# Kernel tuning notes

Hardware: AMD Instinct MI355X
Metric: run time of the kernel (lower is better)

The kernel has to match this reference:

```python
import jax, jax.numpy as jnp
import numpy as np
import math

B, S, D, H, L = 16, 1024, 256, 8, 4
OBS, ACT = 160, 96
DH = D // H  # 32, even as required by RoPE
ROPE_BASE = 10000.0
LN_EPS = 1e-5


def setup_inputs() -> dict:
    key = jax.random.key(0)
    ks = jax.random.split(key, 16)
    s = 0.02
    n = jax.random.normal
    return {
        "obs_seq": n(ks[0], (B, S, OBS), jnp.float32),
        "action_seq": n(ks[1], (B, S, ACT), jnp.float32),
        # linears stored as [in, out] (transpose of torch convention)
        "in_W": n(ks[2], (OBS + ACT, D), jnp.float32) * s,
        "in_b": jnp.zeros((D,), jnp.float32),
        "qW": n(ks[3], (L, D, D), jnp.float32) * s,
        "qb": jnp.zeros((L, D), jnp.float32),
        "kW": n(ks[4], (L, D, D), jnp.float32) * s,
        "kb": jnp.zeros((L, D), jnp.float32),
        "vW": n(ks[5], (L, D, D), jnp.float32) * s,
        "vb": jnp.zeros((L, D), jnp.float32),
        "oW": n(ks[6], (L, D, D), jnp.float32) * s,
        "ob": jnp.zeros((L, D), jnp.float32),
        "out_W": n(ks[7], (D, D), jnp.float32) * s,
        "out_b": jnp.zeros((D,), jnp.float32),
        "ln_g": jnp.ones((D,), jnp.float32),
        "ln_b": jnp.zeros((D,), jnp.float32),
    }


def _rope(x):
    # x: [B,H,S,DH]; interleaved real/imag rotation (stride-2 split like torch code)
    pos = jnp.arange(S, dtype=jnp.float32)[:, None]                 # [S,1]
    freq_seq = jnp.arange(0, DH, 2, dtype=jnp.float32)              # [DH/2]
    inv_freq = 1.0 / (ROPE_BASE ** (freq_seq / DH))
    freqs = pos * inv_freq[None, :]                                  # [S,DH/2]
    cos = jnp.cos(freqs)[None, None]                                 # [1,1,S,DH/2]
    sin = jnp.sin(freqs)[None, None]
    xr = x[..., 0::2]
    xi = x[..., 1::2]
    rr = xr * cos - xi * sin
    ri = xr * sin + xi * cos
    # interleave back: [..., DH/2, 2] -> [..., DH]
    return jnp.stack([rr, ri], axis=-1).reshape(x.shape)


def _attn_layer(x, qW, qb, kW, kb, vW, vb, oW, ob):
    def heads(t):
        return t.reshape(B, S, H, DH).transpose(0, 2, 1, 3)  # [B,H,S,DH]
    q = _rope(heads(x @ qW + qb))
    k = _rope(heads(x @ kW + kb))
    v = heads(x @ vW + vb)
    scores = jnp.einsum('bhqd,bhkd->bhqk', q, k) / math.sqrt(DH)
    w = jax.nn.softmax(scores, axis=-1)  # dropout is identity at inference
    o = jnp.einsum('bhqk,bhkd->bhqd', w, v)
    o = o.transpose(0, 2, 1, 3).reshape(B, S, D)
    return o @ oW + ob


def reference(obs_seq, action_seq, in_W, in_b, qW, qb, kW, kb, vW, vb, oW, ob,
              out_W, out_b, ln_g, ln_b):
    x = jnp.concatenate([obs_seq, action_seq], axis=-1) @ in_W + in_b  # [B,S,D]
    for l in range(L):  # residual self-attention stack with RoPE
        x = x + _attn_layer(x, qW[l], qb[l], kW[l], kb[l], vW[l], vb[l], oW[l], ob[l])
    y = x @ out_W + out_b
    mu = jnp.mean(y, axis=-1, keepdims=True)
    var = jnp.mean(jnp.square(y - mu), axis=-1, keepdims=True)
    y = (y - mu) / jnp.sqrt(var + LN_EPS) * ln_g + ln_b
    context_embedding = y[:, -1]       # seq_lengths=None path: last timestep
    sequence_embeddings = y
    return context_embedding, sequence_embeddings
```

## Files before the change

kernel.cpp:

```cpp
#include <hip/hip_runtime.h>
#include <hip/hip_bf16.h>
#include <math.h>

#define B_ 16
#define S_ 1024
#define D_ 256
#define H_ 8
#define L_ 4
#define DH_ 32
#define OBS_ 160
#define ACT_ 96
#define M_ (B_*S_)

typedef __attribute__((ext_vector_type(8)))  short short8v;
typedef __attribute__((ext_vector_type(4)))  short short4v;
typedef __attribute__((ext_vector_type(4)))  float f32x4;
typedef __attribute__((ext_vector_type(4)))  unsigned uint4v;

#define ALPHA_ 0.25507313f

__device__ inline short bf16rne(float x) {
    unsigned u = __builtin_bit_cast(unsigned, x);
    unsigned r = (u + 0x7fffu + ((u >> 16) & 1u)) >> 16;
    return (short)r;
}

#if __has_builtin(__builtin_amdgcn_exp2f)
#define EXP2F(x) __builtin_amdgcn_exp2f(x)
#else
#define EXP2F(x) exp2f(x)
#endif

__device__ inline unsigned cvtpk_bf16(float lo, float hi) {
    unsigned r;
    asm("v_cvt_pk_bf16_f32 %0, %1, %2" : "=v"(r) : "v"(lo), "v"(hi));
    return r;
}

__global__ __launch_bounds__(256) void rope_table_k(float* __restrict__ cosT2,
                                                    float* __restrict__ sinT2) {
    int idx = blockIdx.x * 256 + threadIdx.x;
    int i = idx >> 10, s = idx & 1023;
    float invf = powf(10000.0f, -(float)(2 * i) / 32.0f);
    float ang = (float)s * invf;
    float sn, cs;
    sincosf(ang, &sn, &cs);
    cosT2[idx] = cs;
    sinT2[idx] = sn;
}

__global__ __launch_bounds__(256) void cvt_in_k(const float* __restrict__ obs,
                                                const float* __restrict__ act,
                                                short* __restrict__ xIn) {
    const int idx = (blockIdx.x * 256 + threadIdx.x) * 8;
    const int row = idx >> 8, col = idx & 255;
    const float* s = (col < OBS_) ? (obs + (size_t)row * OBS_ + col)
                                  : (act + (size_t)row * ACT_ + (col - OBS_));
    const float4 v0 = *(const float4*)s;
    const float4 v1 = *(const float4*)(s + 4);
    short8v o = {bf16rne(v0.x), bf16rne(v0.y), bf16rne(v0.z), bf16rne(v0.w),
                 bf16rne(v1.x), bf16rne(v1.y), bf16rne(v1.z), bf16rne(v1.w)};
    *(short8v*)&xIn[idx] = o;
}

__global__ __launch_bounds__(256) void wconv_k(
    const float* __restrict__ qW, const float* __restrict__ kW,
    const float* __restrict__ vW, const float* __restrict__ oW,
    const float* __restrict__ outW, const float* __restrict__ inW,
    short* __restrict__ WTqkv, short* __restrict__ WTo,
    short* __restrict__ WTf, short* __restrict__ WTin)
{
    __shared__ float T[64][65];
    const int z = blockIdx.y;
    const int bx = blockIdx.x;
    const int tr = (bx & 3) * 64, tc = (bx >> 2) * 64;
    const float* src;
    short* dst;
    if (z < 16) {
        int lay = z >> 2, w = z & 3;
        if (w == 0)      { src = qW + lay * 65536; dst = WTqkv + lay * 196608; }
        else if (w == 1) { src = kW + lay * 65536; dst = WTqkv + lay * 196608 + 65536; }
        else if (w == 2) { src = vW + lay * 65536; dst = WTqkv + lay * 196608 + 131072; }
        else             { src = oW + lay * 65536; dst = WTo + lay * 65536; }
    } else if (z == 16) { src = outW; dst = WTf; }
    else                { src = inW;  dst = WTin; }
    const int tid = threadIdx.x;
    #pragma unroll
    for (int it = 0; it < 4; ++it) {
        int r = (tid >> 4) + it * 16, c = (tid & 15) * 4;
        *(float4*)&T[r][c] = *(const float4*)&src[(size_t)(tr + r) * 256 + tc + c];
    }
    __syncthreads();
    #pragma unroll
    for (int it = 0; it < 4; ++it) {
        int n = (tid >> 4) + it * 16, k = (tid & 15) * 4;
        short4v o = {bf16rne(T[k][n]), bf16rne(T[k + 1][n]),
                     bf16rne(T[k + 2][n]), bf16rne(T[k + 3][n])};
        *(short4v*)&dst[(size_t)(tc + n) * 256 + tr + k] = o;
    }
}

template<int EPI>
__global__ __launch_bounds__(256) void gemm_k(
    const short* __restrict__ A, const short* __restrict__ WT,
    const float* __restrict__ bq, const float* __restrict__ bk,
    const float* __restrict__ bv,
    float* __restrict__ xF, short* __restrict__ xB,
    short* __restrict__ Q2, short* __restrict__ K2, short* __restrict__ VT,
    float* __restrict__ yF,
    const float* __restrict__ cosT2, const float* __restrict__ sinT2)
{
    __shared__ short As[2][128 * 32];
    __shared__ short Bs[2][64 * 32];
    const int tid = threadIdx.x;
    const int l = tid & 63;
    const int wid = tid >> 6, wr = wid >> 1, wc = wid & 1;
    const int bn = blockIdx.x * 64, bm = blockIdx.y * 128;

    const short* aSrc0 = A + (size_t)(bm + (tid >> 2)) * 256 + (tid & 3) * 8;
    const short* aSrc1 = aSrc0 + 64 * 256;
    const short* bSrc  = WT + (size_t)(bn + (tid >> 2)) * 256 + (tid & 3) * 8;

    short8v a0 = *(const short8v*)aSrc0;
    short8v a1 = *(const short8v*)aSrc1;
    short8v b0 = *(const short8v*)bSrc;
    *(short8v*)&As[0][tid * 8]         = a0;
    *(short8v*)&As[0][(tid + 256) * 8] = a1;
    *(short8v*)&Bs[0][tid * 8]         = b0;
    __syncthreads();

    f32x4 acc[4][2];
    #pragma unroll
    for (int i = 0; i < 4; ++i)
        #pragma unroll
        for (int j = 0; j < 2; ++j) acc[i][j] = (f32x4){0.f, 0.f, 0.f, 0.f};

    #pragma unroll
    for (int t = 0; t < 8; ++t) {
        const int cur = t & 1;
        short8v na0, na1, nb;
        if (t < 7) {
            const int k = (t + 1) * 32;
            na0 = *(const short8v*)&aSrc0[k];
            na1 = *(const short8v*)&aSrc1[k];
            nb  = *(const short8v*)&bSrc[k];
        }
        short8v af[4], bf[2];
        #pragma unroll
        for (int i = 0; i < 4; ++i)
            af[i] = *(const short8v*)&As[cur][(wr * 64 + i * 16 + (l & 15)) * 32 + (l >> 4) * 8];
        #pragma unroll
        for (int j = 0; j < 2; ++j)
            bf[j] = *(const short8v*)&Bs[cur][(wc * 32 + j * 16 + (l & 15)) * 32 + (l >> 4) * 8];
        #pragma unroll
        for (int i = 0; i < 4; ++i)
            #pragma unroll
            for (int j = 0; j < 2; ++j)
                acc[i][j] = __builtin_amdgcn_mfma_f32_16x16x32_bf16(af[i], bf[j], acc[i][j], 0, 0, 0);
        if (t < 7) {
            const int nxt = cur ^ 1;
            *(short8v*)&As[nxt][tid * 8]         = na0;
            *(short8v*)&As[nxt][(tid + 256) * 8] = na1;
            *(short8v*)&Bs[nxt][tid * 8]         = nb;
            __syncthreads();
        }
    }

    if (EPI == 0) {
        const int region = bn >> 8;
        if (region == 2) {
            #pragma unroll
            for (int i = 0; i < 4; ++i) {
                const int m0 = bm + wr * 64 + i * 16 + ((l >> 4) << 2);
                const int bI = m0 >> 10, s0 = m0 & 1023;
                const int w  = s0 & 31;
                const int sp = (s0 & ~31) | ((((w & 15) >> 2) << 3) | ((w >> 4) << 2));
                #pragma unroll
                for (int j = 0; j < 2; ++j) {
                    const int nl = (bn & 255) + wc * 32 + j * 16 + (l & 15);
                    const float bb = bv[nl];
                    const f32x4 v = acc[i][j];
                    const int h = nl >> 5, dhh = nl & 31;
                    short4v o = {bf16rne(v[0] + bb), bf16rne(v[1] + bb),
                                 bf16rne(v[2] + bb), bf16rne(v[3] + bb)};
                    *(short4v*)&VT[((size_t)((bI * 8 + h) * 32 + dhh) << 10) + sp] = o;
                }
            }
        } else {
            const float* bias = (region == 0) ? bq : bk;
            __syncthreads();
            short* scr = &As[0][0];
            #pragma unroll
            for (int i = 0; i < 4; ++i) {
                const int tl0 = wr * 64 + i * 16 + ((l >> 4) << 2);
                const int s0r = (bm + tl0) & 1023;
                #pragma unroll
                for (int j = 0; j < 2; ++j) {
                    const int ncl = wc * 32 + j * 16 + (l & 15);
                    const int nl = (bn & 255) + ncl;
                    const float bb = bias[nl];
                    f32x4 v = acc[i][j];
                    v[0] += bb; v[1] += bb; v[2] += bb; v[3] += bb;
                    if (region == 0) { v *= ALPHA_; }
                    const int ir = (nl & 31) >> 1;
                    const f32x4 cs = *(const f32x4*)&cosT2[ir * 1024 + s0r];
                    const f32x4 sn = *(const f32x4*)&sinT2[ir * 1024 + s0r];
                    f32x4 pr;
                    #pragma unroll
                    for (int c = 0; c < 4; ++c) pr[c] = __shfl_xor(v[c], 1);
                    const float sg = (nl & 1) ? 1.f : -1.f;
                    #pragma unroll
                    for (int c = 0; c < 4; ++c)
                        v[c] = v[c] * cs[c] + sg * pr[c] * sn[c];
                    #pragma unroll
                    for (int c = 0; c < 4; ++c) {
                        const int tl = tl0 + c;
                        const int pos = (((ncl >> 3) ^ (tl & 7)) << 3) | (ncl & 7);
                        scr[tl * 64 + pos] = bf16rne(v[c]);
                    }
                }
            }
            __syncthreads();
            const int r = tid >> 1, h2 = tid & 1;
            const int tok = bm + r;
            const int bI = tok >> 10, s0 = tok & 1023;
            const int hh = ((bn & 255) >> 5) + h2;
            short* dst = ((region == 0) ? Q2 : K2)
                         + ((size_t)((bI * 8 + hh) * 1024 + s0)) * 32;
            #pragma unroll
            for (int k = 0; k < 4; ++k) {
                const int pos = ((h2 * 4 + k) ^ (r & 7)) << 3;
                *(uint4*)&dst[k * 8] = *(const uint4*)&scr[r * 64 + pos];
            }
        }
    } else {
        #pragma unroll
        for (int i = 0; i < 4; ++i) {
            const int m0 = bm + wr * 64 + i * 16 + ((l >> 4) << 2);
            #pragma unroll
            for (int j = 0; j < 2; ++j) {
                const int nn = bn + wc * 32 + j * 16 + (l & 15);
                const float bb = bq[nn];
                const f32x4 v = acc[i][j];
                #pragma unroll
                for (int c = 0; c < 4; ++c) {
                    float rr = v[c] + bb;
                    const size_t off = (size_t)(m0 + c) * 256 + nn;
                    if (EPI == 1) rr += xF[off];
                    if (EPI == 3) {
                        yF[off] = rr;
                    } else {
                        xF[off] = rr;
                        xB[off] = bf16rne(rr);
                    }
                }
            }
        }
    }
}

__global__ __launch_bounds__(512, 2) void attn_k(
    const short* __restrict__ Q2, const short* __restrict__ K2,
    const short* __restrict__ VT, short* __restrict__ O)
{
    __shared__ short lb[65536];
    const int tid = threadIdx.x;
    const int l = tid & 63, wid = tid >> 6;
    const int head = blockIdx.x & 127;
    const int qh = blockIdx.x >> 7;
    const int q0w = qh * 512 + wid * 64;
    const int lq = l & 15, g = l >> 4;

    const short* Kh = K2 + (size_t)head * 32768;
    const short* Vh = VT + (size_t)head * 32768;

    #pragma unroll
    for (int i = 0; i < 8; ++i) {
        const int c = tid + i * 512;
        short8v kv = *(const short8v*)(Kh + c * 8);
        const int key = c >> 2, dc = c & 3;
        *(short8v*)((char*)lb + key * 64 + ((dc ^ ((key >> 1) & 3)) << 4)) = kv;
        short8v vv = *(const short8v*)(Vh + c * 8);
        const int dh = c >> 7, kc = c & 127;
        *(short8v*)((char*)lb + 65536 + (kc >> 2) * 2048 + dh * 64
                    + (((kc & 3) ^ ((dh >> 1) & 3)) << 4)) = vv;
    }

    const short* qp = Q2 + ((size_t)head * 1024 + q0w + lq) * 32 + g * 8;
    const short8v QfA = *(const short8v*)qp;
    const short8v QfB = *(const short8v*)(qp + 512);
    const short8v QfC = *(const short8v*)(qp + 1024);
    const short8v QfD = *(const short8v*)(qp + 1536);

    const char* LBK = (const char*)lb + lq * 64 + ((g ^ ((lq >> 1) & 3)) << 4);
    const char* LBV = LBK + 65536;

    f32x4 aA0 = {0.f,0.f,0.f,0.f}, aA1 = {0.f,0.f,0.f,0.f};
    f32x4 aB0 = {0.f,0.f,0.f,0.f}, aB1 = {0.f,0.f,0.f,0.f};
    f32x4 aC0 = {0.f,0.f,0.f,0.f}, aC1 = {0.f,0.f,0.f,0.f};
    f32x4 aD0 = {0.f,0.f,0.f,0.f}, aD1 = {0.f,0.f,0.f,0.f};
    const f32x4 z4 = {0.f, 0.f, 0.f, 0.f};
    float lsA = 0.f, lsB = 0.f, lsC = 0.f, lsD = 0.f;

    __syncthreads();

#define QSTEP(QF, A0, A1, LS) do {                                             \
        f32x4 s0 = __builtin_amdgcn_mfma_f32_16x16x32_bf16(Kf0, QF, z4, 0,0,0);\
        f32x4 s1 = __builtin_amdgcn_mfma_f32_16x16x32_bf16(Kf1, QF, z4, 0,0,0);\
        float p0 = EXP2F(s0[0]), p1 = EXP2F(s0[1]);                            \
        float p2 = EXP2F(s0[2]), p3 = EXP2F(s0[3]);                            \
        float p4 = EXP2F(s1[0]), p5 = EXP2F(s1[1]);                            \
        float p6 = EXP2F(s1[2]), p7 = EXP2F(s1[3]);                            \
        LS += ((p0 + p1) + (p2 + p3)) + ((p4 + p5) + (p6 + p7));               \
        uint4v pv = {cvtpk_bf16(p0, p1), cvtpk_bf16(p2, p3),                   \
                     cvtpk_bf16(p4, p5), cvtpk_bf16(p6, p7)};                  \
        short8v Pf = __builtin_bit_cast(short8v, pv);                          \
        A0 = __builtin_amdgcn_mfma_f32_16x16x32_bf16(Vf0, Pf, A0, 0,0,0);      \
        A1 = __builtin_amdgcn_mfma_f32_16x16x32_bf16(Vf1, Pf, A1, 0,0,0);      \
    } while (0)

    #pragma unroll 4
    for (int t = 0; t < 32; ++t) {
        const short8v Kf0 = *(const short8v*)(LBK + t * 2048);
        const short8v Kf1 = *(const short8v*)(LBK + t * 2048 + 1024);
        const short8v Vf0 = *(const short8v*)(LBV + t * 2048);
        const short8v Vf1 = *(const short8v*)(LBV + t * 2048 + 1024);
        QSTEP(QfA, aA0, aA1, lsA);
        QSTEP(QfB, aB0, aB1, lsB);
        QSTEP(QfC, aC0, aC1, lsC);
        QSTEP(QfD, aD0, aD1, lsD);
    }
#undef QSTEP

    lsA += __shfl_xor(lsA, 16); lsA += __shfl_xor(lsA, 32);
    lsB += __shfl_xor(lsB, 16); lsB += __shfl_xor(lsB, 32);
    lsC += __shfl_xor(lsC, 16); lsC += __shfl_xor(lsC, 32);
    lsD += __shfl_xor(lsD, 16); lsD += __shfl_xor(lsD, 32);
    const int bI = head >> 3, hh = head & 7;
    short* op = O + ((size_t)(bI * 1024 + q0w + lq)) * 256 + hh * 32 + g * 4;
#define QOUT(A0, A1, LS, ROFF) do {                                            \
        const float inv = 1.f / (LS);                                          \
        short4v o0 = {bf16rne(A0[0] * inv), bf16rne(A0[1] * inv),              \
                      bf16rne(A0[2] * inv), bf16rne(A0[3] * inv)};             \
        short4v o1 = {bf16rne(A1[0] * inv), bf16rne(A1[1] * inv),              \
                      bf16rne(A1[2] * inv), bf16rne(A1[3] * inv)};             \
        *(short4v*)(op + (ROFF) * 256) = o0;                                   \
        *(short4v*)(op + (ROFF) * 256 + 16) = o1;                              \
    } while (0)
    QOUT(aA0, aA1, lsA, 0);
    QOUT(aB0, aB1, lsB, 16);
    QOUT(aC0, aC1, lsC, 32);
    QOUT(aD0, aD1, lsD, 48);
#undef QOUT
}

__global__ __launch_bounds__(256) void ln_k(
    const float* __restrict__ y, const float* __restrict__ g,
    const float* __restrict__ bta, float* __restrict__ outp)
{
    const int tid = threadIdx.x;
    const int wave = tid >> 6, lane = tid & 63;
    const int row = blockIdx.x * 4 + wave;
    const int col = lane * 4;
    float4 t = *(const float4*)&y[(size_t)row * 256 + col];
    float sum = t.x + t.y + t.z + t.w;
    float ss  = t.x * t.x + t.y * t.y + t.z * t.z + t.w * t.w;
    #pragma unroll
    for (int off = 32; off; off >>= 1) {
        sum += __shfl_xor(sum, off);
        ss  += __shfl_xor(ss, off);
    }
    float mean = sum * (1.f / 256.f);
    float var  = ss * (1.f / 256.f) - mean * mean;
    float rstd = rsqrtf(var + 1e-5f);
    float4 gv = *(const float4*)&g[col];
    float4 bv = *(const float4*)&bta[col];
    float4 o;
    o.x = (t.x - mean) * rstd * gv.x + bv.x;
    o.y = (t.y - mean) * rstd * gv.y + bv.y;
    o.z = (t.z - mean) * rstd * gv.z + bv.z;
    o.w = (t.w - mean) * rstd * gv.w + bv.w;
    float* seq = outp + B_ * D_;
    *(float4*)&seq[(size_t)row * 256 + col] = o;
    if ((row & (S_ - 1)) == S_ - 1)
        *(float4*)&outp[(size_t)(row >> 10) * 256 + col] = o;
}

extern "C" void kernel_launch(void* const* d_in, const int* in_sizes, int n_in,
                              void* d_out, int out_size, void* d_ws, size_t ws_size,
                              hipStream_t stream)
{
    const float* obs  = (const float*)d_in[0];
    const float* act  = (const float*)d_in[1];
    const float* inW  = (const float*)d_in[2];
    const float* inb  = (const float*)d_in[3];
    const float* qW   = (const float*)d_in[4];
    const float* qb   = (const float*)d_in[5];
    const float* kW   = (const float*)d_in[6];
    const float* kb   = (const float*)d_in[7];
    const float* vW   = (const float*)d_in[8];
    const float* vb   = (const float*)d_in[9];
    const float* oW   = (const float*)d_in[10];
    const float* ob   = (const float*)d_in[11];
    const float* outW = (const float*)d_in[12];
    const float* outb = (const float*)d_in[13];
    const float* lng  = (const float*)d_in[14];
    const float* lnb  = (const float*)d_in[15];
    float* outp = (float*)d_out;

    const size_t MD = (size_t)M_ * D_;
    float* xF    = (float*)d_ws;
    short* xB    = (short*)(xF + MD);
    short* xIn   = xB + MD;
    short* Q2    = xIn + MD;
    short* K2    = Q2 + MD;
    short* VT    = K2 + MD;
    short* Obf   = VT + MD;
    short* WTqkv = Obf + MD;
    short* WTo   = WTqkv + 786432;
    short* WTf   = WTo + 262144;
    short* WTin  = WTf + 65536;
    float* cosT2 = (float*)(WTin + 65536);
    float* sinT2 = cosT2 + 16384;
    float* ybuf  = (float*)Q2;

    rope_table_k<<<64, 256, 0, stream>>>(cosT2, sinT2);
    cvt_in_k<<<2048, 256, 0, stream>>>(obs, act, xIn);
    wconv_k<<<dim3(16, 18), 256, 0, stream>>>(qW, kW, vW, oW, outW, inW,
                                              WTqkv, WTo, WTf, WTin);

    gemm_k<2><<<dim3(4, 128), 256, 0, stream>>>(xIn, WTin, inb, nullptr, nullptr,
            xF, xB, nullptr, nullptr, nullptr, nullptr, nullptr, nullptr);

    for (int lay = 0; lay < L_; ++lay) {
        gemm_k<0><<<dim3(12, 128), 256, 0, stream>>>(xB, WTqkv + lay * 196608,
                qb + lay * 256, kb + lay * 256, vb + lay * 256,
                nullptr, nullptr, Q2, K2, VT, nullptr, cosT2, sinT2);
        attn_k<<<256, 512, 0, stream>>>(Q2, K2, VT, Obf);
        gemm_k<1><<<dim3(4, 128), 256, 0, stream>>>(Obf, WTo + lay * 65536,
                ob + lay * 256, nullptr, nullptr, xF, xB,
                nullptr, nullptr, nullptr, nullptr, nullptr, nullptr);
    }

    gemm_k<3><<<dim3(4, 128), 256, 0, stream>>>(xB, WTf, outb, nullptr, nullptr,
            nullptr, nullptr, nullptr, nullptr, nullptr, ybuf, nullptr, nullptr);
    ln_k<<<M_ / 4, 256, 0, stream>>>(ybuf, lng, lnb, outp);
}
```

Baseline: 309.2 us.

## Load GEMM tiles directly into LDS and merge preprocessing kernels

The GEMM double-buffer loop now uses global_load_lds 16-byte transfers, writing the next K-slice straight into shared memory. This replaces the register round-trip and explicit LDS stores, and also frees registers. Separately, the rope-table, input-convert and weight-transpose kernels are combined into one launch that dispatches on block index, removing two launches. The main risk is that correctness depends on the compiler placing the vmcnt wait before each barrier for the asynchronous LDS writes.

```diff
diff --git a/kernel.cpp b/kernel.cpp
--- a/kernel.cpp
+++ b/kernel.cpp
@@ -37,66 +37,71 @@
     return r;
 }
 
-__global__ __launch_bounds__(256) void rope_table_k(float* __restrict__ cosT2,
-                                                    float* __restrict__ sinT2) {
-    int idx = blockIdx.x * 256 + threadIdx.x;
-    int i = idx >> 10, s = idx & 1023;
-    float invf = powf(10000.0f, -(float)(2 * i) / 32.0f);
-    float ang = (float)s * invf;
-    float sn, cs;
-    sincosf(ang, &sn, &cs);
-    cosT2[idx] = cs;
-    sinT2[idx] = sn;
-}
-
-__global__ __launch_bounds__(256) void cvt_in_k(const float* __restrict__ obs,
-                                                const float* __restrict__ act,
-                                                short* __restrict__ xIn) {
-    const int idx = (blockIdx.x * 256 + threadIdx.x) * 8;
-    const int row = idx >> 8, col = idx & 255;
-    const float* s = (col < OBS_) ? (obs + (size_t)row * OBS_ + col)
-                                  : (act + (size_t)row * ACT_ + (col - OBS_));
-    const float4 v0 = *(const float4*)s;
-    const float4 v1 = *(const float4*)(s + 4);
-    short8v o = {bf16rne(v0.x), bf16rne(v0.y), bf16rne(v0.z), bf16rne(v0.w),
-                 bf16rne(v1.x), bf16rne(v1.y), bf16rne(v1.z), bf16rne(v1.w)};
-    *(short8v*)&xIn[idx] = o;
-}
-
-__global__ __launch_bounds__(256) void wconv_k(
+__device__ __forceinline__ void gload16(const void* g, void* lds) {
+    __builtin_amdgcn_global_load_lds(
+        (const __attribute__((address_space(1))) unsigned*)g,
+        (__attribute__((address_space(3))) unsigned*)lds, 16, 0, 0);
+}
+
+__global__ __launch_bounds__(256) void preproc_k(
+    const float* __restrict__ obs, const float* __restrict__ act,
     const float* __restrict__ qW, const float* __restrict__ kW,
     const float* __restrict__ vW, const float* __restrict__ oW,
     const float* __restrict__ outW, const float* __restrict__ inW,
+    short* __restrict__ xIn,
     short* __restrict__ WTqkv, short* __restrict__ WTo,
-    short* __restrict__ WTf, short* __restrict__ WTin)
+    short* __restrict__ WTf, short* __restrict__ WTin,
+    float* __restrict__ cosT2, float* __restrict__ sinT2)
 {
     __shared__ float T[64][65];
-    const int z = blockIdx.y;
-    const int bx = blockIdx.x;
-    const int tr = (bx & 3) * 64, tc = (bx >> 2) * 64;
-    const float* src;
-    short* dst;
-    if (z < 16) {
-        int lay = z >> 2, w = z & 3;
-        if (w == 0)      { src = qW + lay * 65536; dst = WTqkv + lay * 196608; }
-        else if (w == 1) { src = kW + lay * 65536; dst = WTqkv + lay * 196608 + 65536; }
-        else if (w == 2) { src = vW + lay * 65536; dst = WTqkv + lay * 196608 + 131072; }
-        else             { src = oW + lay * 65536; dst = WTo + lay * 65536; }
-    } else if (z == 16) { src = outW; dst = WTf; }
-    else                { src = inW;  dst = WTin; }
+    const int bid = blockIdx.x;
     const int tid = threadIdx.x;
-    #pragma unroll
-    for (int it = 0; it < 4; ++it) {
-        int r = (tid >> 4) + it * 16, c = (tid & 15) * 4;
-        *(float4*)&T[r][c] = *(const float4*)&src[(size_t)(tr + r) * 256 + tc + c];
-    }
-    __syncthreads();
-    #pragma unroll
-    for (int it = 0; it < 4; ++it) {
-        int n = (tid >> 4) + it * 16, k = (tid & 15) * 4;
-        short4v o = {bf16rne(T[k][n]), bf16rne(T[k + 1][n]),
-                     bf16rne(T[k + 2][n]), bf16rne(T[k + 3][n])};
-        *(short4v*)&dst[(size_t)(tc + n) * 256 + tr + k] = o;
+
+    if (bid < 288) {
+        const int bx = bid & 15, z = bid >> 4;
+        const int tr = (bx & 3) * 64, tc = (bx >> 2) * 64;
+        const float* src;
+        short* dst;
+        if (z < 16) {
+            int lay = z >> 2, w = z & 3;
+            if (w == 0)      { src = qW + lay * 65536; dst = WTqkv + lay * 196608; }
+            else if (w == 1) { src = kW + lay * 65536; dst = WTqkv + lay * 196608 + 65536; }
+            else if (w == 2) { src = vW + lay * 65536; dst = WTqkv + lay * 196608 + 131072; }
+            else             { src = oW + lay * 65536; dst = WTo + lay * 65536; }
+        } else if (z == 16) { src = outW; dst = WTf; }
+        else                { src = inW;  dst = WTin; }
+        #pragma unroll
+        for (int it = 0; it < 4; ++it) {
+            int r = (tid >> 4) + it * 16, c = (tid & 15) * 4;
+            *(float4*)&T[r][c] = *(const float4*)&src[(size_t)(tr + r) * 256 + tc + c];
+        }
+        __syncthreads();
+        #pragma unroll
+        for (int it = 0; it < 4; ++it) {
+            int n = (tid >> 4) + it * 16, k = (tid & 15) * 4;
+            short4v o = {bf16rne(T[k][n]), bf16rne(T[k + 1][n]),
+                         bf16rne(T[k + 2][n]), bf16rne(T[k + 3][n])};
+            *(short4v*)&dst[(size_t)(tc + n) * 256 + tr + k] = o;
+        }
+    } else if (bid < 2336) {
+        const int idx = ((bid - 288) * 256 + tid) * 8;
+        const int row = idx >> 8, col = idx & 255;
+        const float* s = (col < OBS_) ? (obs + (size_t)row * OBS_ + col)
+                                      : (act + (size_t)row * ACT_ + (col - OBS_));
+        const float4 v0 = *(const float4*)s;
+        const float4 v1 = *(const float4*)(s + 4);
+        short8v o = {bf16rne(v0.x), bf16rne(v0.y), bf16rne(v0.z), bf16rne(v0.w),
+                     bf16rne(v1.x), bf16rne(v1.y), bf16rne(v1.z), bf16rne(v1.w)};
+        *(short8v*)&xIn[idx] = o;
+    } else {
+        const int idx = (bid - 2336) * 256 + tid;
+        const int i = idx >> 10, s = idx & 1023;
+        float invf = powf(10000.0f, -(float)(2 * i) / 32.0f);
+        float ang = (float)s * invf;
+        float sn, cs;
+        sincosf(ang, &sn, &cs);
+        cosT2[idx] = cs;
+        sinT2[idx] = sn;
     }
 }
 
@@ -121,12 +126,9 @@
     const short* aSrc1 = aSrc0 + 64 * 256;
     const short* bSrc  = WT + (size_t)(bn + (tid >> 2)) * 256 + (tid & 3) * 8;
 
-    short8v a0 = *(const short8v*)aSrc0;
-    short8v a1 = *(const short8v*)aSrc1;
-    short8v b0 = *(const short8v*)bSrc;
-    *(short8v*)&As[0][tid * 8]         = a0;
-    *(short8v*)&As[0][(tid + 256) * 8] = a1;
-    *(short8v*)&Bs[0][tid * 8]         = b0;
+    gload16(aSrc0, &As[0][tid * 8]);
+    gload16(aSrc1, &As[0][(tid + 256) * 8]);
+    gload16(bSrc,  &Bs[0][tid * 8]);
     __syncthreads();
 
     f32x4 acc[4][2];
@@ -138,12 +140,12 @@
     #pragma unroll
     for (int t = 0; t < 8; ++t) {
         const int cur = t & 1;
-        short8v na0, na1, nb;
         if (t < 7) {
             const int k = (t + 1) * 32;
-            na0 = *(const short8v*)&aSrc0[k];
-            na1 = *(const short8v*)&aSrc1[k];
-            nb  = *(const short8v*)&bSrc[k];
+            const int nxt = cur ^ 1;
+            gload16(aSrc0 + k, &As[nxt][tid * 8]);
+            gload16(aSrc1 + k, &As[nxt][(tid + 256) * 8]);
+            gload16(bSrc + k,  &Bs[nxt][tid * 8]);
         }
         short8v af[4], bf[2];
         #pragma unroll
@@ -157,13 +159,7 @@
             #pragma unroll
             for (int j = 0; j < 2; ++j)
                 acc[i][j] = __builtin_amdgcn_mfma_f32_16x16x32_bf16(af[i], bf[j], acc[i][j], 0, 0, 0);
-        if (t < 7) {
-            const int nxt = cur ^ 1;
-            *(short8v*)&As[nxt][tid * 8]         = na0;
-            *(short8v*)&As[nxt][(tid + 256) * 8] = na1;
-            *(short8v*)&Bs[nxt][tid * 8]         = nb;
-            __syncthreads();
-        }
+        if (t < 7) __syncthreads();
     }
 
     if (EPI == 0) {
@@ -424,10 +420,8 @@
     float* sinT2 = cosT2 + 16384;
     float* ybuf  = (float*)Q2;
 
-    rope_table_k<<<64, 256, 0, stream>>>(cosT2, sinT2);
-    cvt_in_k<<<2048, 256, 0, stream>>>(obs, act, xIn);
-    wconv_k<<<dim3(16, 18), 256, 0, stream>>>(qW, kW, vW, oW, outW, inW,
-                                              WTqkv, WTo, WTf, WTin);
+    preproc_k<<<2400, 256, 0, stream>>>(obs, act, qW, kW, vW, oW, outW, inW,
+                                        xIn, WTqkv, WTo, WTf, WTin, cosT2, sinT2);
 
     gemm_k<2><<<dim3(4, 128), 256, 0, stream>>>(xIn, WTin, inb, nullptr, nullptr,
             xF, xB, nullptr, nullptr, nullptr, nullptr, nullptr, nullptr);
```

Measured after the change: 314.2 us. About the same (+1.6%).
